# Kernel optimization log

Hardware: AMD Instinct MI355X
Metric: run time of the kernel (lower is better)

## Reference

```python
import jax, jax.numpy as jnp
import numpy as np

NUM_EXPERTS = 16
TOP_K = 2


def _swiglu(x, w13, w2):
    # x: [t, d]; w13: [2I, d] (gate and up fused); w2: [d, I]
    h = x @ w13.T                      # [t, 2I]
    gate, up = jnp.split(h, 2, axis=-1)
    return (jax.nn.silu(gate) * up) @ w2.T  # [t, d]


def setup_inputs() -> dict:
    key = jax.random.key(0)
    ks = jax.random.split(key, 6)
    T, D, I, E, SI = 4096, 1024, 512, NUM_EXPERTS, 2048
    return {
        "hidden_states": jax.random.normal(ks[0], (T, D), jnp.float32),
        "router_logits": jax.random.normal(ks[1], (T, E), jnp.float32),
        "w13": jax.random.normal(ks[2], (E, 2 * I, D), jnp.float32) * (1.0 / np.sqrt(D)),
        "w2": jax.random.normal(ks[3], (E, D, I), jnp.float32) * (1.0 / np.sqrt(I)),
        "w13_shared": jax.random.normal(ks[4], (2 * SI, D), jnp.float32) * (1.0 / np.sqrt(D)),
        "w2_shared": jax.random.normal(ks[5], (D, SI), jnp.float32) * (1.0 / np.sqrt(SI)),
    }


def reference(hidden_states, router_logits, w13, w2, w13_shared, w2_shared):
    # Shared expert path (overlapped with routed dispatch in the original).
    shared_out = _swiglu(hidden_states, w13_shared, w2_shared)  # [T, d]

    # Routing: softmax -> top-k -> renormalize (vLLM FusedMoE w/ renormalize=True).
    probs = jax.nn.softmax(router_logits, axis=-1)              # [T, E]
    topk_w, topk_idx = jax.lax.top_k(probs, TOP_K)              # [T, k]
    topk_w = topk_w / jnp.sum(topk_w, axis=-1, keepdims=True)

    # Dense combine-weight matrix [T, E]: zero where expert not selected.
    T = hidden_states.shape[0]
    combine = jnp.zeros((T, NUM_EXPERTS), hidden_states.dtype)
    combine = combine.at[jnp.arange(T)[:, None], topk_idx].add(topk_w)

    # Grouped expert compute: scan over experts (fixed structural set),
    # accumulating the combine-weighted SwiGLU output. Memory-friendly: no
    # [E, T, 2I] intermediate is materialized.
    def body(acc, ew):
        w13_e, w2_e, c_e = ew                     # [2I,d], [d,I], [T]
        y = _swiglu(hidden_states, w13_e, w2_e)   # [T, d]
        return acc + c_e[:, None] * y, None

    fused_out, _ = jax.lax.scan(body, jnp.zeros_like(hidden_states),
                                (w13, w2, combine.T))
    return shared_out, fused_out
```

## Files before the change

### kernel.cpp

```cpp
#include <hip/hip_runtime.h>


#define T_TOK 4096
#define NEXP  16

typedef __attribute__((ext_vector_type(8))) short   short8;
typedef __attribute__((ext_vector_type(4))) float   floatx4;

typedef __attribute__((address_space(1))) void as1_void;
typedef __attribute__((address_space(3))) void as3_void;

__device__ __forceinline__ float bf2f(ushort u) {
    union { unsigned int i; float f; } v; v.i = ((unsigned int)u) << 16; return v.f;
}
__device__ __forceinline__ ushort f2bf(float f) {
    unsigned int u = __builtin_bit_cast(unsigned int, f);
    unsigned int r = 0x7FFFu + ((u >> 16) & 1u);
    return (ushort)((u + r) >> 16);
}

__device__ __forceinline__ float load_elem(const void* p, long i, int bf) {
    return bf ? bf2f(((const ushort*)p)[i]) : ((const float*)p)[i];
}

__global__ void detect_dtype(const ushort* __restrict__ xu, int* __restrict__ dflag) {
    __shared__ int cnt;
    if (threadIdx.x == 0) cnt = 0;
    __syncthreads();
    int ok = 0;
    for (int i = threadIdx.x; i < 512; i += 256) {
        int e = (xu[2 * i] >> 7) & 0xFF;
        ok += (e >= 90 && e <= 140) ? 1 : 0;
    }
    atomicAdd(&cnt, ok);
    __syncthreads();
    if (threadIdx.x == 0) *dflag = (cnt >= 384) ? 1 : 0;
}

__global__ void detect_xsel(const void* __restrict__ p0, const void* __restrict__ p4,
                            const int* __restrict__ dflag, int* __restrict__ xsel) {
    __shared__ float s0s, s4s;
    if (threadIdx.x == 0) { s0s = 0.f; s4s = 0.f; }
    __syncthreads();
    int bf = *dflag;
    float a0 = 0.f, a4 = 0.f;
    for (int i = threadIdx.x; i < 4096; i += 256) {
        a0 += fabsf(load_elem(p0, (long)i * 997 + 13, bf));
        a4 += fabsf(load_elem(p4, (long)i * 997 + 13, bf));
    }
    atomicAdd(&s0s, a0);
    atomicAdd(&s4s, a4);
    __syncthreads();
    if (threadIdx.x == 0) *xsel = (s0s >= s4s) ? 0 : 1;
}

__device__ __forceinline__ void top2(const void* logits, int t, int bf,
                                     int& b0, int& b1, float& w0, float& w1) {
    float l[16];
#pragma unroll
    for (int j = 0; j < 16; ++j) l[j] = load_elem(logits, t * 16 + j, bf);
    b0 = 0; float v0 = l[0];
#pragma unroll
    for (int j = 1; j < 16; ++j) { if (l[j] > v0) { v0 = l[j]; b0 = j; } }
    b1 = -1; float v1 = -3.4e38f;
#pragma unroll
    for (int j = 0; j < 16; ++j) {
        if (j == b0) continue;
        if (l[j] > v1) { v1 = l[j]; b1 = j; }
    }
    float d = __expf(v1 - v0);
    w0 = 1.0f / (1.0f + d);
    w1 = d / (1.0f + d);
}

__global__ void router_counts(const void* __restrict__ logits, const int* __restrict__ dflag,
                              int* __restrict__ counts) {
    int t = blockIdx.x * blockDim.x + threadIdx.x;
    if (t >= T_TOK) return;
    int b0, b1; float w0, w1;
    top2(logits, t, *dflag, b0, b1, w0, w1);
    atomicAdd(&counts[b0], 1);
    atomicAdd(&counts[b1], 1);
}

__global__ void scan_kernel(const int* __restrict__ counts, int* __restrict__ offsets) {
    if (threadIdx.x == 0 && blockIdx.x == 0) {
        int acc = 0;
        for (int e = 0; e < NEXP; ++e) { offsets[e] = acc; acc += counts[e]; }
    }
}

__global__ void router_pairs(const void* __restrict__ logits, const int* __restrict__ dflag,
                             const int* __restrict__ offsets, int* __restrict__ cursor,
                             int* __restrict__ pairinfo, float* __restrict__ pairw) {
    int t = blockIdx.x * blockDim.x + threadIdx.x;
    if (t >= T_TOK) return;
    int b0, b1; float w0, w1;
    top2(logits, t, *dflag, b0, b1, w0, w1);
    int p0 = offsets[b0] + atomicAdd(&cursor[b0], 1);
    pairinfo[p0] = 2 * t;     pairw[p0] = w0;
    int p1 = offsets[b1] + atomicAdd(&cursor[b1], 1);
    pairinfo[p1] = 2 * t + 1; pairw[p1] = w1;
}

__global__ void to_bf16(const void* __restrict__ pA, const void* __restrict__ pB,
                        ushort* __restrict__ dst, long n8,
                        const int* __restrict__ dflag, const int* __restrict__ xsel)
{
    const void* src = (pB != nullptr && *xsel) ? pB : pA;
    const int bf = *dflag;
    long i = (long)blockIdx.x * blockDim.x + threadIdx.x;
    const long stride = (long)gridDim.x * blockDim.x;
    for (; i < n8; i += stride) {
        uint4 v;
        if (bf) {
            v = ((const uint4*)src)[i];
        } else {
            float4 f0 = ((const float4*)src)[i * 2];
            float4 f1 = ((const float4*)src)[i * 2 + 1];
            v.x = (unsigned)f2bf(f0.x) | ((unsigned)f2bf(f0.y) << 16);
            v.y = (unsigned)f2bf(f0.z) | ((unsigned)f2bf(f0.w) << 16);
            v.z = (unsigned)f2bf(f1.x) | ((unsigned)f2bf(f1.y) << 16);
            v.w = (unsigned)f2bf(f1.z) | ((unsigned)f2bf(f1.w) << 16);
        }
        ((uint4*)dst)[i] = v;
    }
}

__device__ __forceinline__ void gload16(const ushort* g, ushort* l) {
    __builtin_amdgcn_global_load_lds((as1_void*)g, (as3_void*)l, 16, 0, 0);
}

template <int SWIGLU, int GATHER, int ROUTED, int SCATTER>
__global__ __launch_bounds__(256)
void gemm_fast(const ushort* __restrict__ A, int lda,
               const ushort* __restrict__ B0, long upoff, long strideB, int ldb,
               void* __restrict__ C, int ldc, float* __restrict__ C2,
               int M, int K,
               const int* __restrict__ counts, const int* __restrict__ offsets,
               const int* __restrict__ pairinfo, const float* __restrict__ pairw)
{
    constexpr int BN  = SWIGLU ? 64 : 128;
    constexpr int NBI = SWIGLU ? 2 : 4;
    constexpr int NFN = SWIGLU ? 2 : 4;

    const int e    = ROUTED ? (int)blockIdx.z : 0;
    const int Mloc = ROUTED ? counts[e] : M;
    const int m0   = blockIdx.y * 128;
    if (m0 >= Mloc) return;
    const int n0   = blockIdx.x * BN;
    const int pair_base = ROUTED ? offsets[e] : 0;
    const long bbase    = ROUTED ? (long)e * strideB : 0L;

    __shared__ __align__(16) ushort As [128 * 64];
    __shared__ __align__(16) ushort Bs0[BN * 64];
    __shared__ __align__(16) ushort Bs1[SWIGLU ? BN * 64 : 8];

    const int tid  = threadIdx.x;
    const int lane = tid & 63;
    const int wave = tid >> 6;
    const int srow = lane >> 3;
    const int scol = (lane & 7) * 8;

    long aoff[4];
#pragma unroll
    for (int i = 0; i < 4; ++i) {
        int rl  = m0 + (wave * 4 + i) * 8 + srow;
        int rlc = rl < Mloc ? rl : Mloc - 1;
        long gr;
        if (GATHER)      gr = (long)(pairinfo[pair_base + rlc] >> 1);
        else if (ROUTED) gr = pair_base + rlc;
        else             gr = rlc;
        aoff[i] = gr * (long)lda + scol;
    }
    long boff[NBI];
#pragma unroll
    for (int i = 0; i < NBI; ++i) {
        int r = (wave * NBI + i) * 8 + srow;
        boff[i] = bbase + (long)(n0 + r) * ldb + scol;
    }

    const int wm   = (wave >> 1) * 64;
    const int wn   = (wave & 1) * (SWIGLU ? 32 : 64);
    const int r16  = lane & 15;
    const int quad = lane >> 4;

    const floatx4 z4 = {0.f, 0.f, 0.f, 0.f};
    floatx4 accg[4][NFN], accu[4][NFN];
#pragma unroll
    for (int mi = 0; mi < 4; ++mi)
#pragma unroll
        for (int ni = 0; ni < NFN; ++ni) { accg[mi][ni] = z4; accu[mi][ni] = z4; }

    for (int k0 = 0; k0 < K; k0 += 64) {
#pragma unroll
        for (int i = 0; i < 4; ++i)
            gload16(A + aoff[i] + k0, &As[(wave * 4 + i) * 512]);
#pragma unroll
        for (int i = 0; i < NBI; ++i) {
            gload16(B0 + boff[i] + k0, &Bs0[(wave * NBI + i) * 512]);
            if constexpr (SWIGLU)
                gload16(B0 + boff[i] + upoff + k0, &Bs1[(wave * NBI + i) * 512]);
        }
        __syncthreads();
#pragma unroll
        for (int kc = 0; kc < 2; ++kc) {
            const int kof = kc * 32 + quad * 8;
            short8 af[4];
#pragma unroll
            for (int mi = 0; mi < 4; ++mi)
                af[mi] = *(const short8*)&As[(wm + mi * 16 + r16) * 64 + kof];
            short8 bfr[NFN], ufr[NFN];
#pragma unroll
            for (int ni = 0; ni < NFN; ++ni) {
                bfr[ni] = *(const short8*)&Bs0[(wn + ni * 16 + r16) * 64 + kof];
                if constexpr (SWIGLU)
                    ufr[ni] = *(const short8*)&Bs1[(wn + ni * 16 + r16) * 64 + kof];
            }
#pragma unroll
            for (int mi = 0; mi < 4; ++mi)
#pragma unroll
                for (int ni = 0; ni < NFN; ++ni) {
                    accg[mi][ni] = __builtin_amdgcn_mfma_f32_16x16x32_bf16(
                        af[mi], bfr[ni], accg[mi][ni], 0, 0, 0);
                    if constexpr (SWIGLU)
                        accu[mi][ni] = __builtin_amdgcn_mfma_f32_16x16x32_bf16(
                            af[mi], ufr[ni], accu[mi][ni], 0, 0, 0);
                }
        }
        __syncthreads();
    }

#pragma unroll
    for (int mi = 0; mi < 4; ++mi) {
#pragma unroll
        for (int r = 0; r < 4; ++r) {
            const int grow = m0 + wm + mi * 16 + quad * 4 + r;
            if (grow >= Mloc) continue;
            int info = 0; float w = 0.f;
            if constexpr (SCATTER) {
                const int p = pair_base + grow;
                info = pairinfo[p]; w = pairw[p];
            }
#pragma unroll
            for (int ni = 0; ni < NFN; ++ni) {
                const int col = n0 + wn + ni * 16 + r16;
                float val;
                if constexpr (SWIGLU) {
                    float g = accg[mi][ni][r];
                    float u = accu[mi][ni][r];
                    val = (g / (1.0f + __expf(-g))) * u;
                } else {
                    val = accg[mi][ni][r];
                }
                if constexpr (SCATTER) {
                    long idx = (long)(info >> 1) * 1024 + col;
                    float* dst = (info & 1) ? C2 : (float*)C;
                    dst[idx] = w * val;
                } else if constexpr (SWIGLU) {
                    long crow = ROUTED ? (long)(pair_base + grow) : (long)grow;
                    ((ushort*)C)[crow * ldc + col] = f2bf(val);
                } else {
                    ((float*)C)[(long)grow * ldc + col] = val;
                }
            }
        }
    }
}

__device__ __forceinline__ void stage8(const void* __restrict__ src, long eoff, int bf,
                                       ushort* __restrict__ dst) {
    if (bf) {
        *(uint4*)dst = *(const uint4*)((const ushort*)src + eoff);
    } else {
        const float* s = (const float*)src + eoff;
        float4 f0 = *(const float4*)s;
        float4 f1 = *(const float4*)(s + 4);
        uint4 v;
        v.x = (unsigned)f2bf(f0.x) | ((unsigned)f2bf(f0.y) << 16);
        v.y = (unsigned)f2bf(f0.z) | ((unsigned)f2bf(f0.w) << 16);
        v.z = (unsigned)f2bf(f1.x) | ((unsigned)f2bf(f1.y) << 16);
        v.w = (unsigned)f2bf(f1.z) | ((unsigned)f2bf(f1.w) << 16);
        *(uint4*)dst = v;
    }
}

template <int SWIGLU, int GATHER, int ROUTED, int SCATTER, int LOCAL,
          int A_DT, int B_DT, int C_F32>
__global__ __launch_bounds__(256)
void gemm_nt(const void* __restrict__ A, const void* __restrict__ Aalt, int lda,
             const void* __restrict__ B0, const void* __restrict__ B0alt,
             long upoff, long strideB,
             void* __restrict__ C, int ldc, void* __restrict__ C2,
             int M, int K, int row0,
             const int* __restrict__ dflag, const int* __restrict__ xsel,
             const int* __restrict__ counts, const int* __restrict__ offsets,
             const int* __restrict__ pairinfo, const float* __restrict__ pairw,
             int e_base, int m_base, int Mcap)
{
    const int dfl = (A_DT && B_DT) ? 1 : *dflag;
    const int abf = A_DT ? 1 : dfl;
    const int bbf = B_DT ? 1 : dfl;
    if (Aalt  && *xsel) A  = Aalt;
    if (B0alt && *xsel) B0 = B0alt;

    const int e = ROUTED ? (e_base + (int)blockIdx.z) : 0;
    int Mloc;
    if (ROUTED) {
        int avail = counts[e] - m_base;
        Mloc = avail < Mcap ? avail : Mcap;
    } else {
        Mloc = M;
    }
    const int m0 = blockIdx.y * 64;
    if (m0 >= Mloc) return;
    const int n0 = blockIdx.x * 64;
    const int pair_base = ROUTED ? (offsets[e] + m_base) : 0;
    const int abase     = ROUTED ? (LOCAL ? 0 : offsets[e]) : 0;
    const long bbase    = ROUTED ? (long)e * strideB : 0L;

    constexpr int LS = 72;
    __shared__ __align__(16) ushort As[64 * LS];
    __shared__ __align__(16) ushort Bs0[64 * LS];
    __shared__ __align__(16) ushort Bs1[SWIGLU ? 64 * LS : 8];

    const int tid = threadIdx.x;

    int  lofs[2];
    long aoff[2], boff[2];
#pragma unroll
    for (int i = 0; i < 2; ++i) {
        int idx = tid + i * 256;
        int row = idx >> 3;
        int col = (idx & 7) * 8;
        lofs[i] = row * LS + col;
        int rl  = m0 + row;
        int rlc = rl < Mloc ? rl : (Mloc - 1);
        long rA;
        if (GATHER)      rA = (long)(pairinfo[pair_base + rlc] >> 1);
        else if (ROUTED) rA = abase + rlc;
        else             rA = row0 + rl;
        aoff[i] = rA * (long)lda + col;
        boff[i] = bbase + (long)(n0 + row) * K + col;
    }

    const int lane = tid & 63;
    const int wave = tid >> 6;
    const int wm   = (wave >> 1) * 32;
    const int wn   = (wave & 1) * 32;
    const int r16  = lane & 15;
    const int quad = lane >> 4;

    floatx4 accg[2][2] = {{{0.f,0.f,0.f,0.f},{0.f,0.f,0.f,0.f}},{{0.f,0.f,0.f,0.f},{0.f,0.f,0.f,0.f}}};
    floatx4 accu[2][2] = {{{0.f,0.f,0.f,0.f},{0.f,0.f,0.f,0.f}},{{0.f,0.f,0.f,0.f},{0.f,0.f,0.f,0.f}}};

    for (int k0 = 0; k0 < K; k0 += 64) {
#pragma unroll
        for (int i = 0; i < 2; ++i) {
            stage8(A,  aoff[i] + k0, abf, &As[lofs[i]]);
            stage8(B0, boff[i] + k0, bbf, &Bs0[lofs[i]]);
            if (SWIGLU) stage8(B0, boff[i] + k0 + upoff, bbf, &Bs1[lofs[i]]);
        }
        __syncthreads();
#pragma unroll
        for (int kc = 0; kc < 2; ++kc) {
            const int kof = kc * 32 + quad * 8;
            short8 a0 = *(const short8*)&As[(wm + r16)      * LS + kof];
            short8 a1 = *(const short8*)&As[(wm + 16 + r16) * LS + kof];
            short8 b0 = *(const short8*)&Bs0[(wn + r16)      * LS + kof];
            short8 b1 = *(const short8*)&Bs0[(wn + 16 + r16) * LS + kof];
            accg[0][0] = __builtin_amdgcn_mfma_f32_16x16x32_bf16(a0, b0, accg[0][0], 0, 0, 0);
            accg[0][1] = __builtin_amdgcn_mfma_f32_16x16x32_bf16(a0, b1, accg[0][1], 0, 0, 0);
            accg[1][0] = __builtin_amdgcn_mfma_f32_16x16x32_bf16(a1, b0, accg[1][0], 0, 0, 0);
            accg[1][1] = __builtin_amdgcn_mfma_f32_16x16x32_bf16(a1, b1, accg[1][1], 0, 0, 0);
            if (SWIGLU) {
                short8 u0 = *(const short8*)&Bs1[(wn + r16)      * LS + kof];
                short8 u1 = *(const short8*)&Bs1[(wn + 16 + r16) * LS + kof];
                accu[0][0] = __builtin_amdgcn_mfma_f32_16x16x32_bf16(a0, u0, accu[0][0], 0, 0, 0);
                accu[0][1] = __builtin_amdgcn_mfma_f32_16x16x32_bf16(a0, u1, accu[0][1], 0, 0, 0);
                accu[1][0] = __builtin_amdgcn_mfma_f32_16x16x32_bf16(a1, u0, accu[1][0], 0, 0, 0);
                accu[1][1] = __builtin_amdgcn_mfma_f32_16x16x32_bf16(a1, u1, accu[1][1], 0, 0, 0);
            }
        }
        __syncthreads();
    }

#pragma unroll
    for (int mi = 0; mi < 2; ++mi) {
#pragma unroll
        for (int ni = 0; ni < 2; ++ni) {
#pragma unroll
            for (int r = 0; r < 4; ++r) {
                int rowl = wm + mi * 16 + quad * 4 + r;
                int grow = m0 + rowl;
                if (grow < Mloc) {
                    int col = n0 + wn + ni * 16 + r16;
                    float g = accg[mi][ni][r];
                    float val;
                    if (SWIGLU) {
                        float u = accu[mi][ni][r];
                        val = (g / (1.0f + __expf(-g))) * u;
                    } else {
                        val = g;
                    }
                    if (SCATTER) {
                        int p    = pair_base + grow;
                        int info = pairinfo[p];
                        float w  = pairw[p];
                        long idx = (long)(info >> 1) * 1024 + col;
                        void* dst = (info & 1) ? C2 : C;
                        if (C_F32) ((float*)dst)[idx]  = w * val;
                        else       ((ushort*)dst)[idx] = f2bf(w * val);
                    } else {
                        int crow = ROUTED ? (abase + grow) : grow;
                        long idx = (long)crow * ldc + col;
                        if (C_F32) ((float*)C)[idx]  = val;
                        else       ((ushort*)C)[idx] = f2bf(val);
                    }
                }
            }
        }
    }
}

__global__ void add_kernel(float* __restrict__ outF, const float* __restrict__ outS, int n4) {
    int i = blockIdx.x * blockDim.x + threadIdx.x;
    if (i >= n4) return;
    float4 a = *(const float4*)(outF + (long)i * 4);
    float4 b = *(const float4*)(outS + (long)i * 4);
    a.x += b.x; a.y += b.y; a.z += b.z; a.w += b.w;
    *(float4*)(outF + (long)i * 4) = a;
}

extern "C" void kernel_launch(void* const* d_in, const int* in_sizes, int n_in,
                              void* d_out, int out_size, void* d_ws, size_t ws_size,
                              hipStream_t stream)
{
    const void* in0  = d_in[0];
    const void* rl   = d_in[1];
    const void* w13  = d_in[2];
    const void* w2   = d_in[3];
    const void* in4  = d_in[4];
    const void* w2s  = d_in[5];
    float* outS = (float*)d_out;
    float* outF = (float*)d_out + (size_t)T_TOK * 1024;

    char*  base     = (char*)d_ws;
    int*   counts   = (int*)(base);
    int*   cursor   = (int*)(base + 64);
    int*   dflag    = (int*)(base + 128);
    int*   xsel     = (int*)(base + 132);
    int*   offsets  = (int*)(base + 192);
    int*   pairinfo = (int*)(base + 256);
    float* pairw    = (float*)(base + 256 + 32768);
    const size_t META = 256 + 65536;

    size_t avail = ws_size > META ? ws_size - META : 0;

    detect_dtype<<<1, 256, 0, stream>>>((const ushort*)in0, dflag);
    detect_xsel<<<1, 256, 0, stream>>>(in0, in4, dflag, xsel);
    hipMemsetAsync(counts, 0, 128, stream);
    router_counts<<<T_TOK / 256, 256, 0, stream>>>(rl, dflag, counts);
    scan_kernel<<<1, 64, 0, stream>>>(counts, offsets);
    router_pairs<<<T_TOK / 256, 256, 0, stream>>>(rl, dflag, offsets, cursor, pairinfo, pairw);

    const long sB1  = (long)1024 * 1024;
    const long sB2  = (long)1024 * 512;
    const long UP_R = (long)512 * 1024;
    const long UP_S = (long)2048 * 1024;

    const size_t FULL_NEED = 88080384ULL;
    const size_t MID_NEED  = 29360128ULL;

    if (avail >= FULL_NEED) {
        ushort* hidb  = (ushort*)(base + META);
        ushort* w13b  = hidb  + (size_t)4096 * 1024;
        ushort* w2b   = w13b  + (size_t)16 * 1024 * 1024;
        ushort* w13sb = w2b   + (size_t)16 * 1024 * 512;
        ushort* w2sb  = w13sb + (size_t)4096 * 1024;
        ushort* actb  = w2sb  + (size_t)1024 * 2048;

        to_bf16<<<1024, 256, 0, stream>>>(in0, in4, hidb,  (long)4096 * 1024 / 8,      dflag, xsel);
        to_bf16<<<1024, 256, 0, stream>>>(w13, nullptr, w13b, (long)16 * 1024 * 1024 / 8, dflag, xsel);
        to_bf16<<<1024, 256, 0, stream>>>(w2,  nullptr, w2b,  (long)16 * 1024 * 512 / 8,  dflag, xsel);
        to_bf16<<<1024, 256, 0, stream>>>(in4, in0, w13sb, (long)4096 * 1024 / 8,      dflag, xsel);
        to_bf16<<<1024, 256, 0, stream>>>(w2s, nullptr, w2sb, (long)1024 * 2048 / 8,      dflag, xsel);

        gemm_fast<1,1,1,0><<<dim3(8, 32, NEXP), 256, 0, stream>>>(
            hidb, 1024, w13b, UP_R, sB1, 1024, actb, 512, nullptr, 0, 1024,
            counts, offsets, pairinfo, pairw);
        gemm_fast<0,0,1,1><<<dim3(8, 32, NEXP), 256, 0, stream>>>(
            actb, 512, w2b, 0, sB2, 512, outF, 1024, outS, 0, 512,
            counts, offsets, pairinfo, pairw);
        add_kernel<<<(T_TOK * 1024 / 4 + 255) / 256, 256, 0, stream>>>(outF, outS, T_TOK * 1024 / 4);
        gemm_fast<1,0,0,0><<<dim3(32, 32), 256, 0, stream>>>(
            hidb, 1024, w13sb, UP_S, 0, 1024, actb, 2048, nullptr, 4096, 1024,
            nullptr, nullptr, nullptr, nullptr);
        gemm_fast<0,0,0,0><<<dim3(8, 32), 256, 0, stream>>>(
            actb, 2048, w2sb, 0, 0, 2048, outS, 1024, nullptr, 4096, 2048,
            nullptr, nullptr, nullptr, nullptr);
    } else if (avail >= MID_NEED) {
        ushort* act   = (ushort*)(base + META);
        ushort* hidb  = act   + (size_t)8192 * 512;
        ushort* w13sb = hidb  + (size_t)4096 * 1024;
        ushort* w2sb  = w13sb + (size_t)4096 * 1024;

        to_bf16<<<1024, 256, 0, stream>>>(in0, in4, hidb,  (long)4096 * 1024 / 8, dflag, xsel);
        to_bf16<<<1024, 256, 0, stream>>>(in4, in0, w13sb, (long)4096 * 1024 / 8, dflag, xsel);
        to_bf16<<<1024, 256, 0, stream>>>(w2s, nullptr, w2sb, (long)1024 * 2048 / 8, dflag, xsel);

        gemm_nt<1,1,1,0,0,1,0,0><<<dim3(8, 64, NEXP), 256, 0, stream>>>(
            hidb, nullptr, 1024, w13, nullptr, UP_R, sB1, act, 512, nullptr, 0, 1024, 0,
            dflag, xsel, counts, offsets, pairinfo, pairw, 0, 0, T_TOK);
        gemm_nt<0,0,1,1,0,1,0,1><<<dim3(16, 64, NEXP), 256, 0, stream>>>(
            act, nullptr, 512, w2, nullptr, 0, sB2, outF, 1024, outS, 0, 512, 0,
            dflag, xsel, counts, offsets, pairinfo, pairw, 0, 0, T_TOK);
        add_kernel<<<(T_TOK * 1024 / 4 + 255) / 256, 256, 0, stream>>>(outF, outS, T_TOK * 1024 / 4);
        for (int c = 0; c < 2; ++c) {
            gemm_fast<1,0,0,0><<<dim3(32, 16), 256, 0, stream>>>(
                hidb + (size_t)c * 2048 * 1024, 1024, w13sb, UP_S, 0, 1024,
                act, 2048, nullptr, 2048, 1024, nullptr, nullptr, nullptr, nullptr);
            gemm_fast<0,0,0,0><<<dim3(8, 16), 256, 0, stream>>>(
                act, 2048, w2sb, 0, 0, 2048, outS + (size_t)c * 2048 * 1024, 1024, nullptr,
                2048, 2048, nullptr, nullptr, nullptr, nullptr);
        }
    } else {
        const size_t MB = 1024 * 1024;
        int grouped, Mcap, CH;
        if      (avail >= 8 * MB) { grouped = 1; Mcap = T_TOK; CH = 2048; }
        else if (avail >= 1 * MB) { grouped = 0; Mcap = 1024;  CH = 256;  }
        else                      { grouped = 0; Mcap = 256;   CH = 64;   }
        ushort* act = (ushort*)(base + META);

        if (grouped) {
            gemm_nt<1,1,1,0,0,0,0,0><<<dim3(8, 64, NEXP), 256, 0, stream>>>(
                in0, in4, 1024, w13, nullptr, UP_R, sB1, act, 512, nullptr, 0, 1024, 0,
                dflag, xsel, counts, offsets, pairinfo, pairw, 0, 0, T_TOK);
            gemm_nt<0,0,1,1,0,1,0,1><<<dim3(16, 64, NEXP), 256, 0, stream>>>(
                act, nullptr, 512, w2, nullptr, 0, sB2, outF, 1024, outS, 0, 512, 0,
                dflag, xsel, counts, offsets, pairinfo, pairw, 0, 0, T_TOK);
        } else {
            for (int e = 0; e < NEXP; ++e) {
                for (int mb = 0; mb < T_TOK; mb += Mcap) {
                    gemm_nt<1,1,1,0,1,0,0,0><<<dim3(8, Mcap / 64, 1), 256, 0, stream>>>(
                        in0, in4, 1024, w13, nullptr, UP_R, sB1, act, 512, nullptr, 0, 1024, 0,
                        dflag, xsel, counts, offsets, pairinfo, pairw, e, mb, Mcap);
                    gemm_nt<0,0,1,1,1,1,0,1><<<dim3(16, Mcap / 64, 1), 256, 0, stream>>>(
                        act, nullptr, 512, w2, nullptr, 0, sB2, outF, 1024, outS, 0, 512, 0,
                        dflag, xsel, counts, offsets, pairinfo, pairw, e, mb, Mcap);
                }
            }
        }
        add_kernel<<<(T_TOK * 1024 / 4 + 255) / 256, 256, 0, stream>>>(outF, outS, T_TOK * 1024 / 4);
        for (int c = 0; c < T_TOK / CH; ++c) {
            gemm_nt<1,0,0,0,0,0,0,0><<<dim3(2048 / 64, CH / 64), 256, 0, stream>>>(
                in0, in4, 1024, in4, in0, UP_S, 0, act, 2048, nullptr, CH, 1024, c * CH,
                dflag, xsel, nullptr, nullptr, nullptr, nullptr, 0, 0, 0);
            gemm_nt<0,0,0,0,0,1,0,1><<<dim3(1024 / 64, CH / 64), 256, 0, stream>>>(
                act, nullptr, 2048, w2s, nullptr, 0, 0,
                outS + (size_t)c * CH * 1024, 1024, nullptr, CH, 2048, 0,
                dflag, xsel, nullptr, nullptr, nullptr, nullptr, 0, 0, 0);
        }
    }
    (void)in_sizes; (void)n_in; (void)out_size;
}
```

Measured before the change: 456.6 us.

## Merge routed and shared expert GEMMs into single launches with swizzled LDS

New measurement: 443.9 us. -2.8%, faster.

```diff
diff --git a/kernel.cpp b/kernel.cpp
--- a/kernel.cpp
+++ b/kernel.cpp
@@ -132,35 +132,26 @@
 }
 
 template <int SWIGLU, int GATHER, int ROUTED, int SCATTER>
-__global__ __launch_bounds__(256)
-void gemm_fast(const ushort* __restrict__ A, int lda,
-               const ushort* __restrict__ B0, long upoff, long strideB, int ldb,
-               void* __restrict__ C, int ldc, float* __restrict__ C2,
-               int M, int K,
-               const int* __restrict__ counts, const int* __restrict__ offsets,
-               const int* __restrict__ pairinfo, const float* __restrict__ pairw)
+__device__ __forceinline__ void gemm_core(
+    ushort* __restrict__ smem,
+    const ushort* __restrict__ A, int lda,
+    const ushort* __restrict__ B0, long upoff, long bbase, int ldb,
+    void* __restrict__ C, int ldc, float* __restrict__ C2,
+    int m0, int n0, int Mloc, int K, int pair_base,
+    const int* __restrict__ pairinfo, const float* __restrict__ pairw)
 {
-    constexpr int BN  = SWIGLU ? 64 : 128;
     constexpr int NBI = SWIGLU ? 2 : 4;
     constexpr int NFN = SWIGLU ? 2 : 4;
 
-    const int e    = ROUTED ? (int)blockIdx.z : 0;
-    const int Mloc = ROUTED ? counts[e] : M;
-    const int m0   = blockIdx.y * 128;
-    if (m0 >= Mloc) return;
-    const int n0   = blockIdx.x * BN;
-    const int pair_base = ROUTED ? offsets[e] : 0;
-    const long bbase    = ROUTED ? (long)e * strideB : 0L;
-
-    __shared__ __align__(16) ushort As [128 * 64];
-    __shared__ __align__(16) ushort Bs0[BN * 64];
-    __shared__ __align__(16) ushort Bs1[SWIGLU ? BN * 64 : 8];
+    ushort* As  = smem;
+    ushort* Bs0 = smem + 128 * 64;
+    ushort* Bs1 = SWIGLU ? (smem + 128 * 64 + 64 * 64) : nullptr;
 
     const int tid  = threadIdx.x;
     const int lane = tid & 63;
     const int wave = tid >> 6;
     const int srow = lane >> 3;
-    const int scol = (lane & 7) * 8;
+    const int scol = ((lane & 7) ^ srow) * 8;
 
     long aoff[4];
 #pragma unroll
@@ -184,6 +175,7 @@
     const int wn   = (wave & 1) * (SWIGLU ? 32 : 64);
     const int r16  = lane & 15;
     const int quad = lane >> 4;
+    const int rlow = r16 & 7;
 
     const floatx4 z4 = {0.f, 0.f, 0.f, 0.f};
     floatx4 accg[4][NFN], accu[4][NFN];
@@ -205,17 +197,17 @@
         __syncthreads();
 #pragma unroll
         for (int kc = 0; kc < 2; ++kc) {
-            const int kof = kc * 32 + quad * 8;
+            const int sw = ((kc * 4 + quad) ^ rlow) * 8;
             short8 af[4];
 #pragma unroll
             for (int mi = 0; mi < 4; ++mi)
-                af[mi] = *(const short8*)&As[(wm + mi * 16 + r16) * 64 + kof];
+                af[mi] = *(const short8*)&As[(wm + mi * 16 + r16) * 64 + sw];
             short8 bfr[NFN], ufr[NFN];
 #pragma unroll
             for (int ni = 0; ni < NFN; ++ni) {
-                bfr[ni] = *(const short8*)&Bs0[(wn + ni * 16 + r16) * 64 + kof];
+                bfr[ni] = *(const short8*)&Bs0[(wn + ni * 16 + r16) * 64 + sw];
                 if constexpr (SWIGLU)
-                    ufr[ni] = *(const short8*)&Bs1[(wn + ni * 16 + r16) * 64 + kof];
+                    ufr[ni] = *(const short8*)&Bs1[(wn + ni * 16 + r16) * 64 + sw];
             }
 #pragma unroll
             for (int mi = 0; mi < 4; ++mi)
@@ -265,6 +257,87 @@
                 }
             }
         }
+    }
+}
+
+template <int SWIGLU, int GATHER, int ROUTED, int SCATTER>
+__global__ __launch_bounds__(256)
+void gemm_fast(const ushort* __restrict__ A, int lda,
+               const ushort* __restrict__ B0, long upoff, long strideB, int ldb,
+               void* __restrict__ C, int ldc, float* __restrict__ C2,
+               int M, int K,
+               const int* __restrict__ counts, const int* __restrict__ offsets,
+               const int* __restrict__ pairinfo, const float* __restrict__ pairw)
+{
+    __shared__ __align__(16) ushort smem[16384];
+    const int e    = ROUTED ? (int)blockIdx.z : 0;
+    const int Mloc = ROUTED ? counts[e] : M;
+    const int m0   = blockIdx.y * 128;
+    if (m0 >= Mloc) return;
+    constexpr int BN = SWIGLU ? 64 : 128;
+    const int n0  = blockIdx.x * BN;
+    const int pb  = ROUTED ? offsets[e] : 0;
+    const long bb = ROUTED ? (long)e * strideB : 0L;
+    gemm_core<SWIGLU, GATHER, ROUTED, SCATTER>(
+        smem, A, lda, B0, upoff, bb, ldb, C, ldc, C2,
+        m0, n0, Mloc, K, pb, pairinfo, pairw);
+}
+
+__global__ __launch_bounds__(256)
+void g1_fused(const ushort* __restrict__ hidb, const ushort* __restrict__ w13b,
+              const ushort* __restrict__ w13sb,
+              ushort* __restrict__ actR, ushort* __restrict__ actS,
+              const int* __restrict__ counts, const int* __restrict__ offsets,
+              const int* __restrict__ pairinfo)
+{
+    __shared__ __align__(16) ushort smem[16384];
+    const int z  = blockIdx.z;
+    const int m0 = blockIdx.y * 128;
+    if (z < 4) {
+        const int e    = z * 4 + ((int)blockIdx.x >> 3);
+        const int Mloc = counts[e];
+        if (m0 >= Mloc) return;
+        const int n0 = ((int)blockIdx.x & 7) * 64;
+        gemm_core<1, 1, 1, 0>(smem, hidb, 1024,
+                              w13b, (long)512 * 1024, (long)e * 1024 * 1024, 1024,
+                              actR, 512, nullptr,
+                              m0, n0, Mloc, 1024, offsets[e], pairinfo, nullptr);
+    } else {
+        const int n0 = (int)blockIdx.x * 64;
+        gemm_core<1, 0, 0, 0>(smem, hidb, 1024,
+                              w13sb, (long)2048 * 1024, 0L, 1024,
+                              actS, 2048, nullptr,
+                              m0, n0, T_TOK, 1024, 0, nullptr, nullptr);
+    }
+}
+
+__global__ __launch_bounds__(256)
+void g2_fused(const ushort* __restrict__ actR, const ushort* __restrict__ actS,
+              const ushort* __restrict__ w2b, const ushort* __restrict__ w2sb,
+              float* __restrict__ outF, float* __restrict__ outT,
+              float* __restrict__ outS,
+              const int* __restrict__ counts, const int* __restrict__ offsets,
+              const int* __restrict__ pairinfo, const float* __restrict__ pairw)
+{
+    __shared__ __align__(16) ushort smem[16384];
+    const int z  = blockIdx.z;
+    const int m0 = blockIdx.y * 128;
+    if (z < 4) {
+        const int e    = z * 4 + ((int)blockIdx.x >> 3);
+        const int Mloc = counts[e];
+        if (m0 >= Mloc) return;
+        const int n0 = ((int)blockIdx.x & 7) * 128;
+        gemm_core<0, 0, 1, 1>(smem, actR, 512,
+                              w2b, 0L, (long)e * 1024 * 512, 512,
+                              outF, 1024, outT,
+                              m0, n0, Mloc, 512, offsets[e], pairinfo, pairw);
+    } else {
+        if ((int)blockIdx.x >= 8) return;
+        const int n0 = (int)blockIdx.x * 128;
+        gemm_core<0, 0, 0, 0>(smem, actS, 2048,
+                              w2sb, 0L, 0L, 2048,
+                              outS, 1024, nullptr,
+                              m0, n0, T_TOK, 2048, 0, nullptr, nullptr);
     }
 }
 
@@ -423,11 +496,11 @@
     }
 }
 
-__global__ void add_kernel(float* __restrict__ outF, const float* __restrict__ outS, int n4) {
+__global__ void add_kernel(float* __restrict__ outF, const float* __restrict__ outT, int n4) {
     int i = blockIdx.x * blockDim.x + threadIdx.x;
     if (i >= n4) return;
     float4 a = *(const float4*)(outF + (long)i * 4);
-    float4 b = *(const float4*)(outS + (long)i * 4);
+    float4 b = *(const float4*)(outT + (long)i * 4);
     a.x += b.x; a.y += b.y; a.z += b.z; a.w += b.w;
     *(float4*)(outF + (long)i * 4) = a;
 }
@@ -469,10 +542,33 @@
     const long UP_R = (long)512 * 1024;
     const long UP_S = (long)2048 * 1024;
 
-    const size_t FULL_NEED = 88080384ULL;
-    const size_t MID_NEED  = 29360128ULL;
-
-    if (avail >= FULL_NEED) {
+    const size_t FULL2_NEED = 96468992ULL;
+    const size_t FULL_NEED  = 88080384ULL;
+    const size_t MID_NEED   = 29360128ULL;
+
+    if (avail >= FULL2_NEED) {
+        ushort* hidb  = (ushort*)(base + META);
+        ushort* w13sb = hidb  + (size_t)4096 * 1024;
+        ushort* w13b  = w13sb + (size_t)4096 * 1024;
+        ushort* w2b   = w13b  + (size_t)16 * 1024 * 1024;
+        ushort* w2sb  = w2b   + (size_t)16 * 1024 * 512;
+        ushort* actR  = w2sb  + (size_t)1024 * 2048;
+        ushort* actS  = actR  + (size_t)8192 * 512;
+        float*  outT  = (float*)hidb;
+
+        to_bf16<<<1024, 256, 0, stream>>>(in0, in4, hidb,  (long)4096 * 1024 / 8,      dflag, xsel);
+        to_bf16<<<1024, 256, 0, stream>>>(in4, in0, w13sb, (long)4096 * 1024 / 8,      dflag, xsel);
+        to_bf16<<<1024, 256, 0, stream>>>(w13, nullptr, w13b, (long)16 * 1024 * 1024 / 8, dflag, xsel);
+        to_bf16<<<1024, 256, 0, stream>>>(w2,  nullptr, w2b,  (long)16 * 1024 * 512 / 8,  dflag, xsel);
+        to_bf16<<<1024, 256, 0, stream>>>(w2s, nullptr, w2sb, (long)1024 * 2048 / 8,      dflag, xsel);
+
+        g1_fused<<<dim3(32, 32, 5), 256, 0, stream>>>(
+            hidb, w13b, w13sb, actR, actS, counts, offsets, pairinfo);
+        g2_fused<<<dim3(32, 32, 5), 256, 0, stream>>>(
+            actR, actS, w2b, w2sb, outF, outT, outS,
+            counts, offsets, pairinfo, pairw);
+        add_kernel<<<(T_TOK * 1024 / 4 + 255) / 256, 256, 0, stream>>>(outF, outT, T_TOK * 1024 / 4);
+    } else if (avail >= FULL_NEED) {
         ushort* hidb  = (ushort*)(base + META);
         ushort* w13b  = hidb  + (size_t)4096 * 1024;
         ushort* w2b   = w13b  + (size_t)16 * 1024 * 1024;
```
